# Kernel optimization log

Measured on AMD Instinct MI355X. Metric: run time of the kernel, lower is better.

The kernel has to match this reference:

```python
import jax, jax.numpy as jnp
import numpy as np

THRESHOLD = 0.5
EPS = 1e-6


def setup_inputs() -> dict:
    key = jax.random.key(0)
    k1, k2 = jax.random.split(key)
    points = jax.random.normal(k1, (16, 10, 30, 2), dtype=jnp.float32)
    polys = jax.random.normal(k2, (16, 16, 200, 2), dtype=jnp.float32)
    return {"points": points, "drivable_multipolygon": polys}


def reference(points, drivable_multipolygon):
    # points: (B, C, T, 2); drivable_multipolygon: (B, K, N, 2)
    # Broadcast layout: (B, K, C, T, N-1, ...)
    ps = drivable_multipolygon[:, :, None, None, :-1, :]   # edge starts (B,K,1,1,N-1,2)
    pe = drivable_multipolygon[:, :, None, None, 1:, :]    # edge ends   (B,K,1,1,N-1,2)
    pts = points[:, None, :, :, None, :]                   # (B,1,C,T,1,2)

    # --- point-to-segment distance ---
    v1 = pts - ps
    ev = pe - ps
    dot = jnp.sum(v1 * ev, axis=-1)
    esq = jnp.sum(ev * ev, axis=-1)
    proj = jnp.clip(dot / (esq + EPS), 0.0, 1.0)
    closest = ev * proj[..., None] + ps
    dist_sq = jnp.maximum(jnp.sum((pts - closest) ** 2, axis=-1), EPS)
    min_dist = jnp.min(jnp.sqrt(dist_sq), axis=-1)         # min over edges N-1 -> (B,K,C,T)
    min_dist = jnp.min(min_dist, axis=1)                   # min over polygons K -> (B,C,T)

    # --- ray-casting inside test (parity of crossings) ---
    py = pts[..., 1]
    px = pts[..., 0]
    sy, sx = ps[..., 1], ps[..., 0]
    ey, ex = pe[..., 1], pe[..., 0]
    cond_y = ((sy <= py) & (py < ey)) | ((ey <= py) & (py < sy))
    slope = (ey - sy) / (ex - sx + EPS)
    intersect_x = sx + (py - sy) / (slope + EPS)
    is_left = intersect_x > px
    intersection = cond_y & is_left                        # (B,K,C,T,N-1)
    crossings = jnp.sum(jnp.sum(intersection.astype(jnp.int32), axis=-1), axis=1)  # (B,C,T)
    inside = (crossings % 2) == 1

    min_dist = jnp.where(inside, -min_dist, min_dist)
    min_dist = jax.nn.relu(min_dist + THRESHOLD)
    return jnp.sum(min_dist, axis=-1)                      # (B, C)
```

## Files before the change

kernel.cpp:

```cpp
#include <hip/hip_runtime.h>
#include <math.h>
#include <float.h>

#define EPS 1e-6f
#define THRESHOLD 0.5f

#define NB 16
#define NPOLY 16
#define NVERT 200
#define NSEG_PER_POLY 199
#define NSEG (NPOLY * NSEG_PER_POLY)
#define NPTB 300
#define NPOINTS 4800
#define NSLICE 64
#define SEG_PER_SLICE 50

__global__ __launch_bounds__(256) void precompute_kernel(
    const float* __restrict__ polys,
    float4* __restrict__ table,
    float* __restrict__ out)
{
    const int idx = blockIdx.x * 256 + threadIdx.x;
    if (idx < 160) out[idx] = 0.0f;
    if (idx >= NB * NSEG) return;

    const int b = idx / NSEG;
    const int s = idx % NSEG;
    const int m = s / NSEG_PER_POLY;
    const int v = s % NSEG_PER_POLY;

    const float2* poly = (const float2*)polys + ((size_t)(b * NPOLY + m) * NVERT);
    const float2 S = poly[v];
    const float2 E = poly[v + 1];

    const float evx = E.x - S.x;
    const float evy = E.y - S.y;
    const float esq = evx * evx + evy * evy;
    const float inv_esq = 1.0f / (esq + EPS);
    const float slope_eps = evy / (evx + EPS) + EPS;

    table[idx * 2]     = make_float4(S.x, S.y, evx, evy);
    table[idx * 2 + 1] = make_float4(inv_esq, slope_eps, E.y, 0.0f);
}

__global__ __launch_bounds__(320) void seg_kernel(
    const float* __restrict__ points,
    const float4* __restrict__ table,
    float* __restrict__ part_dsq,
    int* __restrict__ part_cross)
{
    const int slice = blockIdx.x;
    const int b     = blockIdx.y;
    const int lp    = threadIdx.x;
    const bool active = lp < NPTB;

    const int pidx = b * NPTB + (active ? lp : 0);
    const float2 pt = *(const float2*)(points + (size_t)pidx * 2);
    const float px = pt.x, py = pt.y;

    const float4* tb = table + (size_t)b * NSEG * 2;
    const int s0 = slice * SEG_PER_SLICE;
    const int s1 = (s0 + SEG_PER_SLICE < NSEG) ? s0 + SEG_PER_SLICE : NSEG;

    float min_dsq = FLT_MAX;
    int crossings = 0;

    #pragma unroll 2
    for (int s = s0; s < s1; ++s) {
        const float4 p0 = tb[s * 2];
        const float4 p1 = tb[s * 2 + 1];
        const float sx = p0.x, sy = p0.y, evx = p0.z, evy = p0.w;
        const float inv_esq = p1.x, slope_eps = p1.y, ey = p1.z;

        const float v1x = px - sx;
        const float v1y = py - sy;
        const float dot = v1x * evx + v1y * evy;
        float t = dot * inv_esq;
        t = fminf(fmaxf(t, 0.0f), 1.0f);
        const float dx = px - (evx * t + sx);
        const float dy = py - (evy * t + sy);
        const float dsq = dx * dx + dy * dy;
        min_dsq = fminf(min_dsq, dsq);

        const bool cond_y = (sy <= py) != (ey <= py);
        const float ix = sx + v1y / slope_eps;
        crossings += (cond_y && (ix > px)) ? 1 : 0;
    }

    if (active) {
        const int o = slice * NPOINTS + pidx;
        part_dsq[o]   = min_dsq;
        part_cross[o] = crossings;
    }
}

__global__ __launch_bounds__(256) void final_kernel(
    const float* __restrict__ part_dsq,
    const int* __restrict__ part_cross,
    float* __restrict__ out)
{
    const int p = blockIdx.x * 256 + threadIdx.x;
    if (p >= NPOINTS) return;

    float md = FLT_MAX;
    int c = 0;
    #pragma unroll 8
    for (int k = 0; k < NSLICE; ++k) {
        md = fminf(md, part_dsq[k * NPOINTS + p]);
        c += part_cross[k * NPOINTS + p];
    }

    float d = sqrtf(fmaxf(md, EPS));
    if (c & 1) d = -d;
    const float val = fmaxf(d + THRESHOLD, 0.0f);

    const int b = p / NPTB;
    const int a = (p % NPTB) / 30;
    atomicAdd(out + b * 10 + a, val);
}

extern "C" void kernel_launch(void* const* d_in, const int* in_sizes, int n_in,
                              void* d_out, int out_size, void* d_ws, size_t ws_size,
                              hipStream_t stream) {
    const float* points = (const float*)d_in[0];
    const float* polys  = (const float*)d_in[1];
    float* out = (float*)d_out;

    char* ws = (char*)d_ws;
    float4* table     = (float4*)ws;
    float*  part_dsq  = (float*)(ws + (2u << 20));
    int*    part_cross= (int*)  (ws + (4u << 20));

    const int n_entries = NB * NSEG;
    precompute_kernel<<<(n_entries + 255) / 256, 256, 0, stream>>>(polys, table, out);

    dim3 grid(NSLICE, NB);
    seg_kernel<<<grid, 320, 0, stream>>>(points, table, part_dsq, part_cross);

    final_kernel<<<(NPOINTS + 255) / 256, 256, 0, stream>>>(part_dsq, part_cross, out);
}
```

Baseline: 87.14 us.

## Fuse segment precompute into seg kernel via shared-memory staging

Removes the separate precompute kernel. Each seg_kernel block now computes its own slice of segment parameters, stores them in shared memory, and the inner loop reads from LDS instead of a global table. Zeroing of the output moves into slice-0 blocks of seg_kernel. This drops one kernel launch and a global round trip for the table. In exchange it adds a __syncthreads and some redundant-free per-block setup work.

```diff
diff --git a/kernel.cpp b/kernel.cpp
--- a/kernel.cpp
+++ b/kernel.cpp
@@ -15,60 +15,52 @@
 #define NSLICE 64
 #define SEG_PER_SLICE 50
 
-__global__ __launch_bounds__(256) void precompute_kernel(
+__global__ __launch_bounds__(320) void seg_kernel(
+    const float* __restrict__ points,
     const float* __restrict__ polys,
-    float4* __restrict__ table,
+    float* __restrict__ part_dsq,
+    int* __restrict__ part_cross,
     float* __restrict__ out)
 {
-    const int idx = blockIdx.x * 256 + threadIdx.x;
-    if (idx < 160) out[idx] = 0.0f;
-    if (idx >= NB * NSEG) return;
+    __shared__ float4 lds[SEG_PER_SLICE * 2];
 
-    const int b = idx / NSEG;
-    const int s = idx % NSEG;
-    const int m = s / NSEG_PER_POLY;
-    const int v = s % NSEG_PER_POLY;
-
-    const float2* poly = (const float2*)polys + ((size_t)(b * NPOLY + m) * NVERT);
-    const float2 S = poly[v];
-    const float2 E = poly[v + 1];
-
-    const float evx = E.x - S.x;
-    const float evy = E.y - S.y;
-    const float esq = evx * evx + evy * evy;
-    const float inv_esq = 1.0f / (esq + EPS);
-    const float slope_eps = evy / (evx + EPS) + EPS;
-
-    table[idx * 2]     = make_float4(S.x, S.y, evx, evy);
-    table[idx * 2 + 1] = make_float4(inv_esq, slope_eps, E.y, 0.0f);
-}
-
-__global__ __launch_bounds__(320) void seg_kernel(
-    const float* __restrict__ points,
-    const float4* __restrict__ table,
-    float* __restrict__ part_dsq,
-    int* __restrict__ part_cross)
-{
     const int slice = blockIdx.x;
     const int b     = blockIdx.y;
     const int lp    = threadIdx.x;
     const bool active = lp < NPTB;
 
+    const int s0 = slice * SEG_PER_SLICE;
+    const int s1 = (s0 + SEG_PER_SLICE < NSEG) ? s0 + SEG_PER_SLICE : NSEG;
+    const int nseg = s1 - s0;
+
+    if (lp < nseg) {
+        const int s = s0 + lp;
+        const int m = s / NSEG_PER_POLY;
+        const int v = s % NSEG_PER_POLY;
+        const float2* poly = (const float2*)polys + ((size_t)(b * NPOLY + m) * NVERT);
+        const float2 S = poly[v];
+        const float2 E = poly[v + 1];
+        const float evx = E.x - S.x;
+        const float evy = E.y - S.y;
+        const float esq = evx * evx + evy * evy;
+        const float inv_esq = 1.0f / (esq + EPS);
+        const float slope_eps = evy / (evx + EPS) + EPS;
+        lds[lp * 2]     = make_float4(S.x, S.y, evx, evy);
+        lds[lp * 2 + 1] = make_float4(inv_esq, slope_eps, E.y, 0.0f);
+    }
+    __syncthreads();
+
     const int pidx = b * NPTB + (active ? lp : 0);
     const float2 pt = *(const float2*)(points + (size_t)pidx * 2);
     const float px = pt.x, py = pt.y;
-
-    const float4* tb = table + (size_t)b * NSEG * 2;
-    const int s0 = slice * SEG_PER_SLICE;
-    const int s1 = (s0 + SEG_PER_SLICE < NSEG) ? s0 + SEG_PER_SLICE : NSEG;
 
     float min_dsq = FLT_MAX;
     int crossings = 0;
 
     #pragma unroll 2
-    for (int s = s0; s < s1; ++s) {
-        const float4 p0 = tb[s * 2];
-        const float4 p1 = tb[s * 2 + 1];
+    for (int j = 0; j < nseg; ++j) {
+        const float4 p0 = lds[j * 2];
+        const float4 p1 = lds[j * 2 + 1];
         const float sx = p0.x, sy = p0.y, evx = p0.z, evy = p0.w;
         const float inv_esq = p1.x, slope_eps = p1.y, ey = p1.z;
 
@@ -91,6 +83,8 @@
         const int o = slice * NPOINTS + pidx;
         part_dsq[o]   = min_dsq;
         part_cross[o] = crossings;
+    } else if (slice == 0 && lp >= NPTB && lp < NPTB + 10) {
+        out[b * 10 + (lp - NPTB)] = 0.0f;
     }
 }
 
@@ -127,15 +121,10 @@
     float* out = (float*)d_out;
 
     char* ws = (char*)d_ws;
-    float4* table     = (float4*)ws;
-    float*  part_dsq  = (float*)(ws + (2u << 20));
-    int*    part_cross= (int*)  (ws + (4u << 20));
-
-    const int n_entries = NB * NSEG;
-    precompute_kernel<<<(n_entries + 255) / 256, 256, 0, stream>>>(polys, table, out);
+    float* part_dsq   = (float*)ws;
+    int*   part_cross = (int*)(ws + (2u << 20));
 
     dim3 grid(NSLICE, NB);
-    seg_kernel<<<grid, 320, 0, stream>>>(points, table, part_dsq, part_cross);
-
+    seg_kernel<<<grid, 320, 0, stream>>>(points, polys, part_dsq, part_cross, out);
     final_kernel<<<(NPOINTS + 255) / 256, 256, 0, stream>>>(part_dsq, part_cross, out);
 }
```

New measurement: 82.95 us. 1.05x faster.
